# Kernel optimization log

Hardware: AMD Instinct MI355X
Metric: run time of the kernel (lower is better)

The kernel has to match this reference:

```python
import jax, jax.numpy as jnp
import numpy as np
import math

NUM_HEADS = 16
HIDDEN = 1024
MLP = 4096
SEQ = 2048
HEAD_DIM = HIDDEN // NUM_HEADS  # 64
EPS = 1e-5


def setup_inputs() -> dict:
    key = jax.random.key(0)
    ks = jax.random.split(key, 16)
    s = 0.02
    inp = {
        "x": jax.random.normal(ks[0], (SEQ, HIDDEN), jnp.float32),
        "rope_cos": jnp.cos(jnp.arange(SEQ, dtype=jnp.float32)[:, None] * (1.0 / (10000.0 ** (jnp.arange(HEAD_DIM // 2, dtype=jnp.float32) * 2 / HEAD_DIM)))[None, :]),
        "rope_sin": jnp.sin(jnp.arange(SEQ, dtype=jnp.float32)[:, None] * (1.0 / (10000.0 ** (jnp.arange(HEAD_DIM // 2, dtype=jnp.float32) * 2 / HEAD_DIM)))[None, :]),
        "norm0_w": jnp.ones((HIDDEN,), jnp.float32),
        "norm0_b": jnp.zeros((HIDDEN,), jnp.float32),
        "norm1_w": jnp.ones((HIDDEN,), jnp.float32),
        "norm1_b": jnp.zeros((HIDDEN,), jnp.float32),
        "wqkv_w": jax.random.normal(ks[1], (3 * HIDDEN, HIDDEN), jnp.float32) * s,
        "wqkv_b": jnp.zeros((3 * HIDDEN,), jnp.float32),
        "wo_w": jax.random.normal(ks[2], (HIDDEN, HIDDEN), jnp.float32) * s,
        "wo_b": jnp.zeros((HIDDEN,), jnp.float32),
        "up_w": jax.random.normal(ks[3], (MLP, HIDDEN), jnp.float32) * s,
        "up_b": jnp.zeros((MLP,), jnp.float32),
        "down_w": jax.random.normal(ks[4], (HIDDEN, MLP), jnp.float32) * s,
        "down_b": jnp.zeros((HIDDEN,), jnp.float32),
        # 4 packed sequences of length 512 each
        "input_row_offsets": jnp.array([0, 512, 1024, 1536, 2048], jnp.int32),
    }
    return inp


def _layernorm(x, w, b):
    m = jnp.mean(x, axis=-1, keepdims=True)
    v = jnp.mean((x - m) ** 2, axis=-1, keepdims=True)
    return (x - m) * jax.lax.rsqrt(v + EPS) * w + b


def _rope(t, cos, sin):
    # t: [S, nh, hd]; cos/sin: [S, hd/2] -> complex rotation of adjacent pairs
    S, nh, hd = t.shape
    t2 = t.reshape(S, nh, hd // 2, 2)
    re, im = t2[..., 0], t2[..., 1]
    c = cos[:, None, :]
    s = sin[:, None, :]
    out = jnp.stack([re * c - im * s, re * s + im * c], axis=-1)
    return out.reshape(S, nh, hd)


def _block(x, rope_cos, rope_sin, norm0_w, norm0_b, wqkv_w, wqkv_b, wo_w, wo_b,
           up_w, up_b, down_w, down_b, norm1_w, norm1_b, input_row_offsets):
    S, H = x.shape
    nh, hd = NUM_HEADS, HEAD_DIM
    h = _layernorm(x, norm0_w, norm0_b)
    qkv = (h @ wqkv_w.T + wqkv_b).reshape(S, 3, nh, hd)
    q, k, v = qkv[:, 0], qkv[:, 1], qkv[:, 2]
    q = _rope(q, rope_cos, rope_sin)
    k = _rope(k, rope_cos, rope_sin)
    # block-diagonal bool mask added as 0/1 float (matches torch `attn_weight += bool_mask`)
    seg = jnp.searchsorted(input_row_offsets, jnp.arange(S), side="right") - 1
    mask = (seg[:, None] == seg[None, :]).astype(jnp.float32)  # [S, S]
    scores = jnp.einsum("shd,thd->hst", q, k) / math.sqrt(hd) + mask[None]
    attn = jax.nn.softmax(scores.astype(jnp.float32), axis=-1).astype(q.dtype)
    out = jnp.einsum("hst,thd->shd", attn, v).reshape(S, H)
    x = x + (out @ wo_w.T + wo_b)
    h = _layernorm(x, norm1_w, norm1_b)
    h = jax.nn.gelu(h @ up_w.T + up_b, approximate=True)
    return x + (h @ down_w.T + down_b)


def reference(x, rope_cos, rope_sin, norm0_w, norm0_b, norm1_w, norm1_b,
              wqkv_w, wqkv_b, wo_w, wo_b, up_w, up_b, down_w, down_b,
              input_row_offsets):
    return _block(x, rope_cos, rope_sin, norm0_w, norm0_b, wqkv_w, wqkv_b,
                  wo_w, wo_b, up_w, up_b, down_w, down_b, norm1_w, norm1_b,
                  input_row_offsets)
```

## Files before the change

kernel.cpp:

```cpp
#include <hip/hip_runtime.h>
#include <hip/hip_bf16.h>
#include <math.h>

#define SEQ 2048
#define HID 1024
#define NH 16
#define HD 64

using f32x4  = __attribute__((ext_vector_type(4))) float;
using bf16x8 = __attribute__((ext_vector_type(8))) short;

union U8 { unsigned int u[4]; bf16x8 v; short s[8]; };

__device__ __forceinline__ short f2bf(float f) {
  unsigned int x = __float_as_uint(f);
  unsigned int r = (x + 0x7fffu + ((x >> 16) & 1u)) >> 16;
  return (short)(r & 0xffffu);
}

__device__ __forceinline__ unsigned int pkbf(float a, float b) {
  return ((unsigned int)(unsigned short)f2bf(a)) |
         (((unsigned int)(unsigned short)f2bf(b)) << 16);
}

__device__ __forceinline__ float bf2f_lo(unsigned int u) {
  return __uint_as_float((u & 0xffffu) << 16);
}
__device__ __forceinline__ float bf2f_hi(unsigned int u) {
  return __uint_as_float(u & 0xffff0000u);
}

__device__ __forceinline__ float fast_exp2(float x) {
#if __has_builtin(__builtin_amdgcn_exp2f)
  return __builtin_amdgcn_exp2f(x);
#else
  return exp2f(x);
#endif
}

__device__ __forceinline__ float fast_rcp(float x) {
#if __has_builtin(__builtin_amdgcn_rcpf)
  return __builtin_amdgcn_rcpf(x);
#else
  return 1.0f / x;
#endif
}

__device__ __forceinline__ float gelu_f(float v) {
  float t = v * (1.5957691216057308f + 0.07135481283942279f * v * v);
  float e = fast_exp2(t * -1.4426950408889634f);
  return v * fast_rcp(1.0f + e);
}

__device__ __forceinline__ void async_cp16(const void* g, void* l) {
  __builtin_amdgcn_global_load_lds(
      (__attribute__((address_space(1))) void*)(g),
      (__attribute__((address_space(3))) void*)(l), 16, 0, 0);
}

__global__ __launch_bounds__(256) void cvtln_kernel(
    const float* __restrict__ a, const float* __restrict__ b,
    const float* __restrict__ c, const float* __restrict__ d,
    short* __restrict__ oa, short* __restrict__ ob,
    short* __restrict__ oc, short* __restrict__ od,
    const float* __restrict__ x, const float* __restrict__ w,
    const float* __restrict__ bb, short* __restrict__ h0) {
  int tid = threadIdx.x;
  if (blockIdx.x < 2048) {
    int row = blockIdx.x;
    float4 v = ((const float4*)(x + (size_t)row * HID))[tid];
    float s  = v.x + v.y + v.z + v.w;
    float s2 = v.x*v.x + v.y*v.y + v.z*v.z + v.w*v.w;
#pragma unroll
    for (int o = 32; o >= 1; o >>= 1) {
      s  += __shfl_xor(s,  o);
      s2 += __shfl_xor(s2, o);
    }
    __shared__ float red[8];
    int wv = tid >> 6;
    if ((tid & 63) == 0) { red[wv] = s; red[4 + wv] = s2; }
    __syncthreads();
    float ts  = red[0] + red[1] + red[2] + red[3];
    float ts2 = red[4] + red[5] + red[6] + red[7];
    float mean = ts * (1.0f / HID);
    float var  = ts2 * (1.0f / HID) - mean * mean;
    float rs = rsqrtf(var + 1e-5f);
    float4 wv4 = ((const float4*)w)[tid];
    float4 bv4 = ((const float4*)bb)[tid];
    short4 o;
    o.x = f2bf((v.x - mean) * rs * wv4.x + bv4.x);
    o.y = f2bf((v.y - mean) * rs * wv4.y + bv4.y);
    o.z = f2bf((v.z - mean) * rs * wv4.z + bv4.z);
    o.w = f2bf((v.w - mean) * rs * wv4.w + bv4.w);
    ((short4*)(h0 + (size_t)row * HID))[tid] = o;
    return;
  }
  int i = (blockIdx.x - 2048) * 256 + tid;
  const float* src; short* dst; int off;
  if (i < 786432)        { src = a; dst = oa; off = i; }
  else if (i < 1048576)  { src = b; dst = ob; off = i - 786432; }
  else if (i < 2097152)  { src = c; dst = oc; off = i - 1048576; }
  else                   { src = d; dst = od; off = i - 2097152; }
  float4 v = ((const float4*)src)[off];
  short4 o;
  o.x = f2bf(v.x); o.y = f2bf(v.y); o.z = f2bf(v.z); o.w = f2bf(v.w);
  ((short4*)dst)[off] = o;
}

__global__ __launch_bounds__(256) void ropev_kernel(const short* __restrict__ qkvb,
    const float* __restrict__ cosb, const float* __restrict__ sinb,
    short* __restrict__ Qh, short* __restrict__ Kh, short* __restrict__ Vt) {
  __shared__ short tile[64 * 72];
  int s0   = blockIdx.x * 64;
  int head = blockIdx.y;
  int tid  = threadIdx.x;
#pragma unroll
  for (int p = 0; p < 2; p++) {
    int seg = p * 256 + tid;
    int row = seg >> 3;
    int c8  = seg & 7;
    bf16x8 v = *(const bf16x8*)(qkvb + (size_t)(s0 + row) * 3072 + 2048 + head * 64 + c8 * 8);
    *(bf16x8*)(tile + row * 72 + c8 * 8) = v;
  }
  int sl = tid >> 3;
  int c  = tid & 7;
#pragma unroll
  for (int j = 0; j < 2; j++) {
    float scale = (j == 0) ? 0.18033688011112043f : 1.0f;
    short* dstm = (j == 0) ? Qh : Kh;
#pragma unroll
    for (int half = 0; half < 2; half++) {
      int s = s0 + half * 32 + sl;
      uint4 uu = *(const uint4*)(qkvb + (size_t)s * 3072 + j * 1024 + head * 64 + c * 8);
      float4 cs = *(const float4*)(cosb + s * 32 + c * 4);
      float4 sn = *(const float4*)(sinb + s * 32 + c * 4);
      uint4 oo;
      {
        float a = bf2f_lo(uu.x), b = bf2f_hi(uu.x);
        oo.x = pkbf(scale * (a * cs.x - b * sn.x), scale * (a * sn.x + b * cs.x));
        a = bf2f_lo(uu.y); b = bf2f_hi(uu.y);
        oo.y = pkbf(scale * (a * cs.y - b * sn.y), scale * (a * sn.y + b * cs.y));
        a = bf2f_lo(uu.z); b = bf2f_hi(uu.z);
        oo.z = pkbf(scale * (a * cs.z - b * sn.z), scale * (a * sn.z + b * cs.z));
        a = bf2f_lo(uu.w); b = bf2f_hi(uu.w);
        oo.w = pkbf(scale * (a * cs.w - b * sn.w), scale * (a * sn.w + b * cs.w));
      }
      *(uint4*)(dstm + ((size_t)head * SEQ + s) * HD + c * 8) = oo;
    }
  }
  __syncthreads();
#pragma unroll
  for (int p = 0; p < 2; p++) {
    int seg = p * 256 + tid;
    int d   = seg >> 3;
    int sc  = seg & 7;
    U8 o;
#pragma unroll
    for (int jj = 0; jj < 8; jj++) o.s[jj] = tile[(sc * 8 + jj) * 72 + d];
    *(bf16x8*)(Vt + ((size_t)head * HD + d) * SEQ + s0 + sc * 8) = o.v;
  }
}

template <int EPI>
__global__ __launch_bounds__(512) void gemm_bt_kernel(
    const short* __restrict__ A, const short* __restrict__ B,
    const float* __restrict__ bias, const float* __restrict__ resid,
    void* __restrict__ outp, int M, int N, int Klen, int Kstride,
    int cx, int cy, int ncx, int ncy, int cz) {
  __shared__ __attribute__((aligned(16))) short Alds[2 * 128 * 64];
  __shared__ __attribute__((aligned(16))) short Blds[2 * 128 * 64];
  int tid = threadIdx.x;
  int w    = tid >> 6;
  int lane = tid & 63;
  int lcol  = lane & 15;
  int lhalf = lane >> 4;

  int xcd = blockIdx.x & 7;
  int lid = blockIdx.x >> 3;
  int cix = xcd % ncx;
  int tt  = xcd / ncx;
  int ciy = tt % ncy;
  int ciz = tt / ncy;
  int xx  = cix * cx + lid % cx;
  int rr  = lid / cx;
  int yy  = ciy * cy + rr % cy;
  int z   = ciz * cz + rr / cy;

  int m0 = yy * 128;
  int n0 = xx * 128;
  int wm = (w & 1) * 64;
  int wn = (w >> 1) * 32;

  const short* apt[2];
  const short* bpt[2];
#pragma unroll
  for (int p = 0; p < 2; p++) {
    int seg = p * 512 + tid;
    int row = seg >> 3;
    int c   = (seg & 7) ^ (row & 7);
    apt[p] = A + (size_t)z * Klen + (size_t)(m0 + row) * Kstride + c * 8;
    bpt[p] = B + (size_t)z * Klen + (size_t)(n0 + row) * Kstride + c * 8;
  }

  f32x4 acc[4][2];
#pragma unroll
  for (int i = 0; i < 4; i++)
#pragma unroll
    for (int j = 0; j < 2; j++) acc[i][j] = (f32x4){0.f, 0.f, 0.f, 0.f};

  int nk = Klen >> 6;
#pragma unroll
  for (int p = 0; p < 2; p++) {
    async_cp16(apt[p], Alds + p * 4096 + w * 512);  apt[p] += 64;
    async_cp16(bpt[p], Blds + p * 4096 + w * 512);  bpt[p] += 64;
  }
  for (int kt = 0; kt < nk; ++kt) {
    int cur = kt & 1;
    const short* Ab = Alds + cur * 8192;
    const short* Bb = Blds + cur * 8192;
    if (kt + 1 < nk) {
      int nb = (cur ^ 1) * 8192;
#pragma unroll
      for (int p = 0; p < 2; p++) {
        async_cp16(apt[p], Alds + nb + p * 4096 + w * 512);  apt[p] += 64;
        async_cp16(bpt[p], Blds + nb + p * 4096 + w * 512);  bpt[p] += 64;
      }
      asm volatile("s_waitcnt vmcnt(4)" ::: "memory");
    } else {
      asm volatile("s_waitcnt vmcnt(0)" ::: "memory");
    }
    __builtin_amdgcn_s_barrier();
    __builtin_amdgcn_sched_barrier(0);
#pragma unroll
    for (int kc = 0; kc < 2; kc++) {
      bf16x8 af[4], bfr[2];
#pragma unroll
      for (int i = 0; i < 4; i++) {
        int row = wm + i * 16 + lcol;
        af[i] = *(const bf16x8*)(Ab + row * 64 + (((kc * 4 + lhalf) ^ (row & 7)) * 8));
      }
#pragma unroll
      for (int j = 0; j < 2; j++) {
        int row = wn + j * 16 + lcol;
        bfr[j] = *(const bf16x8*)(Bb + row * 64 + (((kc * 4 + lhalf) ^ (row & 7)) * 8));
      }
#pragma unroll
      for (int i = 0; i < 4; i++)
#pragma unroll
        for (int j = 0; j < 2; j++)
          acc[i][j] = __builtin_amdgcn_mfma_f32_16x16x32_bf16(af[i], bfr[j], acc[i][j], 0, 0, 0);
    }
    __builtin_amdgcn_s_barrier();
    __builtin_amdgcn_sched_barrier(0);
  }

#pragma unroll
  for (int i = 0; i < 4; i++) {
#pragma unroll
    for (int j = 0; j < 2; j++) {
#pragma unroll
      for (int r = 0; r < 4; r++) {
        int row = m0 + wm + i * 16 + lhalf * 4 + r;
        int col = n0 + wn + j * 16 + lcol;
        float v = acc[i][j][r];
        if (EPI != 5) v += bias[col];
        if (EPI == 2) {
          v = gelu_f(v);
          ((short*)outp)[(size_t)row * N + col] = f2bf(v);
        } else if (EPI == 3) {
          ((short*)outp)[(size_t)row * N + col] = f2bf(v);
        } else {
          ((short*)outp)[(size_t)z * M * N + (size_t)row * N + col] = f2bf(v);
        }
      }
    }
  }
}

__global__ __launch_bounds__(256) void attn_kernel(
    const short* __restrict__ Qh, const short* __restrict__ Kh,
    const short* __restrict__ Vt, const int* __restrict__ offs,
    short* __restrict__ Opart, float* __restrict__ Lpart) {
  __shared__ __attribute__((aligned(16))) short Klds[64 * 64];
  __shared__ __attribute__((aligned(16))) short Vlds[64 * 64];
  __shared__ __attribute__((aligned(16))) unsigned int Plds[4][16 * 34];
  int head = blockIdx.y;
  int q0   = blockIdx.x * 64;
  int z    = blockIdx.z;
  int tid  = threadIdx.x;
  int w    = tid >> 6;
  int lane = tid & 63;
  int lcol = lane & 15;
  int h    = lane >> 4;
  int s7   = lcol & 7;
  int o1 = offs[1], o2 = offs[2], o3 = offs[3];

  int qrow = q0 + w * 16 + lcol;
  const short* qb = Qh + ((size_t)head * SEQ + qrow) * HD;
  bf16x8 qf0 = *(const bf16x8*)(qb + h * 8);
  bf16x8 qf1 = *(const bf16x8*)(qb + 32 + h * 8);
  int sq = (qrow >= o1) + (qrow >= o2) + (qrow >= o3);
  U8 qe;
  qe.u[0] = 0; qe.u[1] = 0; qe.u[2] = 0; qe.u[3] = 0;
  if (h == 0) qe.s[sq] = (short)0x3FB9;

  bf16x8 ones;
#pragma unroll
  for (int i = 0; i < 8; i++) ones[i] = 0x3F80;

  int kb0 = lcol * 64 + ((h ^ s7) * 8);
  int kb1 = lcol * 64 + (((4 + h) ^ s7) * 8);
  int vb0 = kb0, vb1 = kb1;
  int pwb = lcol * 34 + h * 2;
  int prb = lcol * 34 + h * 4;

  int tbeg = z * 512;
  const short* kp0; const short* kp1; const short* vp0; const short* vp1;
  int ld0, ld1;
  {
    int seg = tid, row = seg >> 3, g = (seg & 7) ^ (row & 7);
    kp0 = Kh + ((size_t)head * SEQ + tbeg + row) * HD + g * 8;
    vp0 = Vt + ((size_t)head * HD + row) * SEQ + tbeg + g * 8;
    seg = 256 + tid; row = seg >> 3; g = (seg & 7) ^ (row & 7);
    kp1 = Kh + ((size_t)head * SEQ + tbeg + row) * HD + g * 8;
    vp1 = Vt + ((size_t)head * HD + row) * SEQ + tbeg + g * 8;
    ld0 = w * 512 + lane * 8;
    ld1 = 2048 + w * 512 + lane * 8;
  }

  f32x4 o_acc[4];
#pragma unroll
  for (int nt = 0; nt < 4; nt++) o_acc[nt] = (f32x4){0.f, 0.f, 0.f, 0.f};
  f32x4 acc_l = (f32x4){0.f, 0.f, 0.f, 0.f};

  async_cp16(kp0, Klds + w * 512);          kp0 += 64 * HD;
  async_cp16(kp1, Klds + 2048 + w * 512);   kp1 += 64 * HD;
  async_cp16(vp0, Vlds + w * 512);          vp0 += 64;
  async_cp16(vp1, Vlds + 2048 + w * 512);   vp1 += 64;
  __syncthreads();

  for (int t = 0; t < 8; ++t) {
    bf16x8 krA, krB, vrA, vrB;
    if (t < 7) {
      krA = *(const bf16x8*)kp0;  kp0 += 64 * HD;
      krB = *(const bf16x8*)kp1;  kp1 += 64 * HD;
      vrA = *(const bf16x8*)vp0;  vp0 += 64;
      vrB = *(const bf16x8*)vp1;  vp1 += 64;
      __builtin_amdgcn_sched_barrier(0);
    }
    int t0 = t * 64;

#pragma unroll
    for (int n = 0; n < 4; n++) {
      bf16x8 kf0 = *(const bf16x8*)(Klds + n * 1024 + kb0);
      bf16x8 kf1 = *(const bf16x8*)(Klds + n * 1024 + kb1);
      int key = tbeg + t0 + n * 16 + lcol;
      int sk = (key >= o1) + (key >= o2) + (key >= o3);
      U8 ke;
      ke.u[0] = (h == 0) ? ((sk == 0) ? 0x00003F80u : (sk == 1) ? 0x3F800000u : 0u) : 0u;
      ke.u[1] = (h == 0) ? ((sk == 2) ? 0x00003F80u : (sk == 3) ? 0x3F800000u : 0u) : 0u;
      ke.u[2] = 0; ke.u[3] = 0;

      f32x4 sacc = (f32x4){0.f, 0.f, 0.f, 0.f};
      sacc = __builtin_amdgcn_mfma_f32_16x16x32_bf16(kf0, qf0, sacc, 0, 0, 0);
      sacc = __builtin_amdgcn_mfma_f32_16x16x32_bf16(kf1, qf1, sacc, 0, 0, 0);
      sacc = __builtin_amdgcn_mfma_f32_16x16x32_bf16(ke.v, qe.v, sacc, 0, 0, 0);

      float p0 = fast_exp2(sacc[0]);
      float p1 = fast_exp2(sacc[1]);
      float p2 = fast_exp2(sacc[2]);
      float p3 = fast_exp2(sacc[3]);
      uint2 pw;
      pw.x = __builtin_amdgcn_perm(__float_as_uint(p1), __float_as_uint(p0), 0x07060302);
      pw.y = __builtin_amdgcn_perm(__float_as_uint(p3), __float_as_uint(p2), 0x07060302);
      *(uint2*)&Plds[w][pwb + n * 8] = pw;
    }

#pragma unroll
    for (int kc = 0; kc < 2; kc++) {
      uint2 a = *(const uint2*)&Plds[w][prb + kc * 16];
      uint2 b = *(const uint2*)&Plds[w][prb + kc * 16 + 2];
      U8 pu;
      pu.u[0] = a.x; pu.u[1] = a.y; pu.u[2] = b.x; pu.u[3] = b.y;
      int vb = kc ? vb1 : vb0;
#pragma unroll
      for (int nt = 0; nt < 4; nt++) {
        bf16x8 vf = *(const bf16x8*)(Vlds + nt * 1024 + vb);
        o_acc[nt] = __builtin_amdgcn_mfma_f32_16x16x32_bf16(vf, pu.v, o_acc[nt], 0, 0, 0);
      }
      acc_l = __builtin_amdgcn_mfma_f32_16x16x32_bf16(ones, pu.v, acc_l, 0, 0, 0);
    }
    __syncthreads();
    if (t < 7) {
      *(bf16x8*)(Klds + ld0) = krA;
      *(bf16x8*)(Klds + ld1) = krB;
      *(bf16x8*)(Vlds + ld0) = vrA;
      *(bf16x8*)(Vlds + ld1) = vrB;
    }
    __syncthreads();
  }

  short* op = Opart + ((size_t)z * SEQ + qrow) * HID + head * HD + h * 4;
#pragma unroll
  for (int nt = 0; nt < 4; nt++) {
    uint2 ua;
    ua.x = pkbf(o_acc[nt][0], o_acc[nt][1]);
    ua.y = pkbf(o_acc[nt][2], o_acc[nt][3]);
    *(uint2*)(op + nt * 16) = ua;
  }
  if (lane < 16)
    Lpart[((size_t)z * NH + head) * SEQ + qrow] = acc_l[0];
}

__global__ __launch_bounds__(256) void attn_merge_kernel(
    const short* __restrict__ Opart, const float* __restrict__ Lpart,
    short* __restrict__ attn) {
  int i = blockIdx.x * blockDim.x + threadIdx.x;
  int col4 = i & 255;
  int row  = i >> 8;
  int head = col4 >> 4;
  float acc0 = 0.f, acc1 = 0.f, acc2 = 0.f, acc3 = 0.f, l = 0.f;
#pragma unroll
  for (int zz = 0; zz < 4; zz++) {
    uint2 p = ((const uint2*)(Opart + (size_t)zz * SEQ * HID))[i];
    acc0 += bf2f_lo(p.x); acc1 += bf2f_hi(p.x);
    acc2 += bf2f_lo(p.y); acc3 += bf2f_hi(p.y);
    l += Lpart[((size_t)zz * NH + head) * SEQ + row];
  }
  float rl = fast_rcp(l);
  uint2 o;
  o.x = pkbf(acc0 * rl, acc1 * rl);
  o.y = pkbf(acc2 * rl, acc3 * rl);
  ((uint2*)attn)[i] = o;
}

__global__ __launch_bounds__(256) void merge_ln_kernel(
    const short* __restrict__ part, const float* __restrict__ bias,
    const float* __restrict__ resid, const float* __restrict__ w,
    const float* __restrict__ b, float* __restrict__ x1, short* __restrict__ h1) {
  int row = blockIdx.x;
  int tid = threadIdx.x;
  size_t idx = (size_t)row * HID / 4 + tid;
  float4 v = {0.f, 0.f, 0.f, 0.f};
#pragma unroll
  for (int z = 0; z < 4; z++) {
    uint2 p = ((const uint2*)(part + (size_t)z * SEQ * HID))[idx];
    v.x += bf2f_lo(p.x); v.y += bf2f_hi(p.x);
    v.z += bf2f_lo(p.y); v.w += bf2f_hi(p.y);
  }
  float4 bi = ((const float4*)bias)[tid];
  float4 rs4 = ((const float4*)(resid + (size_t)row * HID))[tid];
  v.x += bi.x + rs4.x; v.y += bi.y + rs4.y; v.z += bi.z + rs4.z; v.w += bi.w + rs4.w;
  ((float4*)(x1 + (size_t)row * HID))[tid] = v;
  float s  = v.x + v.y + v.z + v.w;
  float s2 = v.x*v.x + v.y*v.y + v.z*v.z + v.w*v.w;
#pragma unroll
  for (int o = 32; o >= 1; o >>= 1) {
    s  += __shfl_xor(s,  o);
    s2 += __shfl_xor(s2, o);
  }
  __shared__ float red[8];
  int wv = tid >> 6;
  if ((tid & 63) == 0) { red[wv] = s; red[4 + wv] = s2; }
  __syncthreads();
  float ts  = red[0] + red[1] + red[2] + red[3];
  float ts2 = red[4] + red[5] + red[6] + red[7];
  float mean = ts * (1.0f / HID);
  float var  = ts2 * (1.0f / HID) - mean * mean;
  float rsq = rsqrtf(var + 1e-5f);
  float4 wv4 = ((const float4*)w)[tid];
  float4 bv4 = ((const float4*)b)[tid];
  short4 o;
  o.x = f2bf((v.x - mean) * rsq * wv4.x + bv4.x);
  o.y = f2bf((v.y - mean) * rsq * wv4.y + bv4.y);
  o.z = f2bf((v.z - mean) * rsq * wv4.z + bv4.z);
  o.w = f2bf((v.w - mean) * rsq * wv4.w + bv4.w);
  ((short4*)(h1 + (size_t)row * HID))[tid] = o;
}

__global__ __launch_bounds__(256) void merge_bias_kernel(
    const short* __restrict__ part, const float* __restrict__ bias,
    const float* __restrict__ resid, float* __restrict__ out) {
  int i = blockIdx.x * blockDim.x + threadIdx.x;
  int col4 = i & 255;
  float4 v = {0.f, 0.f, 0.f, 0.f};
#pragma unroll
  for (int z = 0; z < 4; z++) {
    uint2 p = ((const uint2*)(part + (size_t)z * SEQ * HID))[i];
    v.x += bf2f_lo(p.x); v.y += bf2f_hi(p.x);
    v.z += bf2f_lo(p.y); v.w += bf2f_hi(p.y);
  }
  float4 bi = ((const float4*)bias)[col4];
  float4 rs = ((const float4*)resid)[i];
  float4 o;
  o.x = v.x + bi.x + rs.x;
  o.y = v.y + bi.y + rs.y;
  o.z = v.z + bi.z + rs.z;
  o.w = v.w + bi.w + rs.w;
  ((float4*)out)[i] = o;
}

extern "C" void kernel_launch(void* const* d_in, const int* in_sizes, int n_in,
                              void* d_out, int out_size, void* d_ws, size_t ws_size,
                              hipStream_t stream) {
  const float* x      = (const float*)d_in[0];
  const float* ropec  = (const float*)d_in[1];
  const float* ropes  = (const float*)d_in[2];
  const float* n0w    = (const float*)d_in[3];
  const float* n0b    = (const float*)d_in[4];
  const float* n1w    = (const float*)d_in[5];
  const float* n1b    = (const float*)d_in[6];
  const float* wqkv_w = (const float*)d_in[7];
  const float* wqkv_b = (const float*)d_in[8];
  const float* wo_w   = (const float*)d_in[9];
  const float* wo_b   = (const float*)d_in[10];
  const float* up_w   = (const float*)d_in[11];
  const float* up_b   = (const float*)d_in[12];
  const float* down_w = (const float*)d_in[13];
  const float* down_b = (const float*)d_in[14];
  const int*   offs   = (const int*)d_in[15];
  float* out = (float*)d_out;

  char* base = (char*)d_ws;
  short* wqkv_bf = (short*)(base + 0);
  short* wo_bf   = (short*)(base + 6291456);
  short* up_bf   = (short*)(base + 8388608);
  short* down_bf = (short*)(base + 16777216);
  short* h0      = (short*)(base + 25165824);
  short* qkv_bf  = (short*)(base + 29360128);
  short* Qh      = (short*)(base + 41943040);
  short* Kh      = (short*)(base + 46137344);
  short* Vt      = (short*)(base + 50331648);
  short* Opart   = (short*)(base + 54525952);
  float* Lpart   = (float*)(base + 71303168);
  short* attn    = (short*)(base + 71827456);
  float* x1      = (float*)(base + 76021760);
  short* h1      = (short*)(base + 84410368);
  short* wopart  = (short*)(base + 25165824);
  short* u       = (short*)(base + 25165824);
  short* dnpart  = (short*)(base + 41943040);

  cvtln_kernel<<<14336, 256, 0, stream>>>(wqkv_w, wo_w, up_w, down_w,
                                          wqkv_bf, wo_bf, up_bf, down_bf,
                                          x, n0w, n0b, h0);
  gemm_bt_kernel<3><<<384, 512, 0, stream>>>(h0, wqkv_bf, wqkv_b, nullptr,
                                             qkv_bf, 2048, 3072, 1024, 1024,
                                             6, 8, 4, 2, 1);
  ropev_kernel<<<dim3(32, 16), 256, 0, stream>>>(qkv_bf, ropec, ropes, Qh, Kh, Vt);
  attn_kernel<<<dim3(32, 16, 4), 256, 0, stream>>>(Qh, Kh, Vt, offs, Opart, Lpart);
  attn_merge_kernel<<<2048, 256, 0, stream>>>(Opart, Lpart, attn);
  gemm_bt_kernel<5><<<512, 512, 0, stream>>>(attn, wo_bf, nullptr, nullptr,
                                             wopart, 2048, 1024, 256, 1024,
                                             8, 8, 1, 2, 1);
  merge_ln_kernel<<<2048, 256, 0, stream>>>(wopart, wo_b, x, n1w, n1b, x1, h1);
  gemm_bt_kernel<2><<<512, 512, 0, stream>>>(h1, up_bf, up_b, nullptr,
                                             u, 2048, 4096, 1024, 1024,
                                             8, 8, 4, 2, 1);
  gemm_bt_kernel<5><<<512, 512, 0, stream>>>(u, down_bf, nullptr, nullptr,
                                             dnpart, 2048, 1024, 1024, 4096,
                                             8, 8, 1, 2, 1);
  merge_bias_kernel<<<2048, 256, 0, stream>>>(dnpart, down_b, x1, out);
}
```

Before: 259.9 us.

## Add 256x128-tile triple-buffered GEMM kernel for QKV, up and down projections

Adds a new GEMM kernel with 256x128 output tiles, a three-stage async LDS pipeline, and global loads interleaved into the MFMA phases. It is used for the QKV, MLP-up and MLP-down projections in place of the 128x128 double-buffered kernel. Larger tiles raise arithmetic intensity and cut operand reloads, and the deeper pipeline is meant to hide load latency better. In exchange it uses about 144KB of LDS and more accumulator registers, and launches fewer blocks (192 or 256 on a 256-CU part), which can leave CUs idle or make the tail uneven.

```diff
diff --git a/kernel.cpp b/kernel.cpp
--- a/kernel.cpp
+++ b/kernel.cpp
@@ -158,6 +158,152 @@
 #pragma unroll
     for (int jj = 0; jj < 8; jj++) o.s[jj] = tile[(sc * 8 + jj) * 72 + d];
     *(bf16x8*)(Vt + ((size_t)head * HD + d) * SEQ + s0 + sc * 8) = o.v;
+  }
+}
+
+template <int EPI>
+__global__ __launch_bounds__(512) void gemm256_kernel(
+    const short* __restrict__ A, const short* __restrict__ B,
+    const float* __restrict__ bias, void* __restrict__ outp,
+    int M, int N, int Klen, int Kstride,
+    int cx, int cy, int ncx, int ncy) {
+  __shared__ __attribute__((aligned(16))) short Abuf[3 * 256 * 64];
+  __shared__ __attribute__((aligned(16))) short Bbuf[3 * 128 * 64];
+  int tid  = threadIdx.x;
+  int w    = tid >> 6;
+  int lane = tid & 63;
+  int lcol  = lane & 15;
+  int lhalf = lane >> 4;
+  int wm2  = w & 1;
+  int wn4  = w >> 1;
+
+  int xcd = blockIdx.x & 7;
+  int lid = blockIdx.x >> 3;
+  int cix = xcd % ncx;
+  int tt  = xcd / ncx;
+  int ciy = tt % ncy;
+  int ciz = tt / ncy;
+  int xx  = cix * cx + lid % cx;
+  int rr  = lid / cx;
+  int yy  = ciy * cy + rr % cy;
+  int z   = ciz + rr / cy;
+
+  int m0 = yy * 256;
+  int n0 = xx * 128;
+
+  const short* Ast[4]; int Ald[4];
+#pragma unroll
+  for (int p = 0; p < 4; p++) {
+    int seg = p * 512 + tid;
+    int row = seg >> 3;
+    int c   = (seg & 7) ^ (row & 7);
+    Ast[p] = A + (size_t)z * Klen + (size_t)(m0 + row) * Kstride + c * 8;
+    Ald[p] = seg * 8;
+  }
+  const short* Bst[2]; int Bld[2];
+#pragma unroll
+  for (int p = 0; p < 2; p++) {
+    int seg = p * 512 + tid;
+    int row = seg >> 3;
+    int c   = (seg & 7) ^ (row & 7);
+    Bst[p] = B + (size_t)z * Klen + (size_t)(n0 + row) * Kstride + c * 8;
+    Bld[p] = seg * 8;
+  }
+
+  f32x4 acc[8][2];
+#pragma unroll
+  for (int i = 0; i < 8; i++)
+#pragma unroll
+    for (int j = 0; j < 2; j++) acc[i][j] = (f32x4){0.f, 0.f, 0.f, 0.f};
+
+  int nk = Klen >> 6;
+#pragma unroll
+  for (int p = 0; p < 4; p++) { async_cp16(Ast[p], Abuf + Ald[p]); Ast[p] += 64; }
+#pragma unroll
+  for (int p = 0; p < 2; p++) { async_cp16(Bst[p], Bbuf + Bld[p]); Bst[p] += 64; }
+#pragma unroll
+  for (int p = 0; p < 4; p++) { async_cp16(Ast[p], Abuf + 16384 + Ald[p]); Ast[p] += 64; }
+#pragma unroll
+  for (int p = 0; p < 2; p++) { async_cp16(Bst[p], Bbuf + 8192 + Bld[p]); Bst[p] += 64; }
+  asm volatile("s_waitcnt vmcnt(6)" ::: "memory");
+  __builtin_amdgcn_s_barrier();
+  __builtin_amdgcn_sched_barrier(0);
+
+  for (int g = 0; g < nk; ++g) {
+    int cbuf = g % 3;
+    int sbuf = (g + 2) % 3;
+    bool do_stage = (g + 2 < nk);
+    const short* Ab = Abuf + cbuf * 16384;
+    const short* Bb = Bbuf + cbuf * 8192;
+    short* Asd = Abuf + sbuf * 16384;
+    short* Bsd = Bbuf + sbuf * 8192;
+#pragma unroll
+    for (int ph = 0; ph < 4; ++ph) {
+      if (do_stage) {
+        if (ph == 0)      { async_cp16(Ast[0], Asd + Ald[0]); async_cp16(Ast[1], Asd + Ald[1]); }
+        else if (ph == 1) { async_cp16(Ast[2], Asd + Ald[2]); async_cp16(Ast[3], Asd + Ald[3]); }
+        else if (ph == 2) { async_cp16(Bst[0], Bsd + Bld[0]); }
+        else              { async_cp16(Bst[1], Bsd + Bld[1]); }
+      }
+      int mh = ph & 1;
+      int j  = ph >> 1;
+      bf16x8 bf[2], af[4][2];
+#pragma unroll
+      for (int kc = 0; kc < 2; kc++) {
+        int brow = wn4 * 32 + j * 16 + lcol;
+        bf[kc] = *(const bf16x8*)(Bb + brow * 64 + (((kc * 4 + lhalf) ^ (brow & 7)) * 8));
+      }
+#pragma unroll
+      for (int ii = 0; ii < 4; ii++) {
+#pragma unroll
+        for (int kc = 0; kc < 2; kc++) {
+          int arow = wm2 * 128 + (mh * 4 + ii) * 16 + lcol;
+          af[ii][kc] = *(const bf16x8*)(Ab + arow * 64 + (((kc * 4 + lhalf) ^ (arow & 7)) * 8));
+        }
+      }
+#pragma unroll
+      for (int ii = 0; ii < 4; ii++)
+#pragma unroll
+        for (int kc = 0; kc < 2; kc++)
+          acc[mh * 4 + ii][j] = __builtin_amdgcn_mfma_f32_16x16x32_bf16(
+              af[ii][kc], bf[kc], acc[mh * 4 + ii][j], 0, 0, 0);
+      __builtin_amdgcn_sched_barrier(0);
+    }
+    if (do_stage) {
+#pragma unroll
+      for (int p = 0; p < 4; p++) Ast[p] += 64;
+#pragma unroll
+      for (int p = 0; p < 2; p++) Bst[p] += 64;
+      asm volatile("s_waitcnt vmcnt(6)" ::: "memory");
+    } else if (g + 1 < nk) {
+      asm volatile("s_waitcnt vmcnt(0)" ::: "memory");
+    }
+    if (g + 1 < nk) {
+      __builtin_amdgcn_s_barrier();
+      __builtin_amdgcn_sched_barrier(0);
+    }
+  }
+
+#pragma unroll
+  for (int i = 0; i < 8; i++) {
+#pragma unroll
+    for (int j = 0; j < 2; j++) {
+#pragma unroll
+      for (int r = 0; r < 4; r++) {
+        int row = m0 + wm2 * 128 + i * 16 + lhalf * 4 + r;
+        int col = n0 + wn4 * 32 + j * 16 + lcol;
+        float v = acc[i][j][r];
+        if (EPI != 5) v += bias[col];
+        if (EPI == 2) {
+          v = gelu_f(v);
+          ((short*)outp)[(size_t)row * N + col] = f2bf(v);
+        } else if (EPI == 3) {
+          ((short*)outp)[(size_t)row * N + col] = f2bf(v);
+        } else {
+          ((short*)outp)[(size_t)z * M * N + (size_t)row * N + col] = f2bf(v);
+        }
+      }
+    }
   }
 }
 
@@ -543,9 +689,9 @@
   cvtln_kernel<<<14336, 256, 0, stream>>>(wqkv_w, wo_w, up_w, down_w,
                                           wqkv_bf, wo_bf, up_bf, down_bf,
                                           x, n0w, n0b, h0);
-  gemm_bt_kernel<3><<<384, 512, 0, stream>>>(h0, wqkv_bf, wqkv_b, nullptr,
-                                             qkv_bf, 2048, 3072, 1024, 1024,
-                                             6, 8, 4, 2, 1);
+  gemm256_kernel<3><<<192, 512, 0, stream>>>(h0, wqkv_bf, wqkv_b, qkv_bf,
+                                             2048, 3072, 1024, 1024,
+                                             3, 8, 8, 1);
   ropev_kernel<<<dim3(32, 16), 256, 0, stream>>>(qkv_bf, ropec, ropes, Qh, Kh, Vt);
   attn_kernel<<<dim3(32, 16, 4), 256, 0, stream>>>(Qh, Kh, Vt, offs, Opart, Lpart);
   attn_merge_kernel<<<2048, 256, 0, stream>>>(Opart, Lpart, attn);
@@ -553,11 +699,11 @@
                                              wopart, 2048, 1024, 256, 1024,
                                              8, 8, 1, 2, 1);
   merge_ln_kernel<<<2048, 256, 0, stream>>>(wopart, wo_b, x, n1w, n1b, x1, h1);
-  gemm_bt_kernel<2><<<512, 512, 0, stream>>>(h1, up_bf, up_b, nullptr,
-                                             u, 2048, 4096, 1024, 1024,
-                                             8, 8, 4, 2, 1);
-  gemm_bt_kernel<5><<<512, 512, 0, stream>>>(u, down_bf, nullptr, nullptr,
-                                             dnpart, 2048, 1024, 1024, 4096,
-                                             8, 8, 1, 2, 1);
+  gemm256_kernel<2><<<256, 512, 0, stream>>>(h1, up_bf, up_b, u,
+                                             2048, 4096, 1024, 1024,
+                                             4, 8, 8, 1);
+  gemm256_kernel<5><<<256, 512, 0, stream>>>(u, down_bf, nullptr, dnpart,
+                                             2048, 1024, 1024, 4096,
+                                             4, 8, 2, 1);
   merge_bias_kernel<<<2048, 256, 0, stream>>>(dnpart, down_b, x1, out);
 }
```

After: 306.0 us. 17.7% more time.
